# Kernel tuning notes

Measured on AMD Instinct MI355X. Metric: run time of the kernel, lower is better.

## Reference

```python
import jax, jax.numpy as jnp
import numpy as np

BATCH = 1024
LATENT = 16
IMG = 3 * 96 * 96  # 27648


def setup_inputs() -> dict:
    key = jax.random.key(0)
    ks = jax.random.split(key, 16)
    w = lambda k, shape, s=0.05: (jax.random.normal(k, shape, jnp.float32) * s)
    return {
        "x": jax.random.normal(ks[0], (BATCH, 96, 96, 3), jnp.float32),
        "eps_noise": jax.random.normal(ks[1], (BATCH, LATENT), jnp.float32),
        "enc_w1": w(ks[2], (IMG, 900)),
        "enc_b1": jnp.zeros((900,), jnp.float32),
        "enc_w2": w(ks[3], (900, 300)),
        "enc_b2": jnp.zeros((300,), jnp.float32),
        "logvar_w": w(ks[4], (300, LATENT)),
        "logvar_b": jnp.zeros((LATENT,), jnp.float32),
        "W": w(ks[5], (LATENT, LATENT), 0.1),  # nn.init.normal_(std=0.1)
        "dec_w1": w(ks[6], (LATENT, 300)),
        "dec_b1": jnp.zeros((300,), jnp.float32),
        "dec_w2": w(ks[7], (300, 300)),
        "dec_b2": jnp.zeros((300,), jnp.float32),
        "dec_w3": w(ks[8], (300, IMG)),
        "dec_b3": jnp.zeros((IMG,), jnp.float32),
    }


def reference(x, eps_noise, enc_w1, enc_b1, enc_w2, enc_b2, logvar_w, logvar_b,
              W, dec_w1, dec_b1, dec_w2, dec_b2, dec_w3, dec_b3):
    # encoder
    xf = x.reshape(x.shape[0], -1)                      # [B, 27648]
    h = jax.nn.elu(xf @ enc_w1 + enc_b1)
    h = jax.nn.elu(h @ enc_w2 + enc_b2)
    logvar = h @ logvar_w + logvar_b                    # [B, d]

    d = W.shape[0]
    idx = jnp.arange(d, dtype=W.dtype)
    relu_y = jnp.maximum(idx[None, :] - idx[:, None], 0.0)  # ReLU(j - i), strictly upper tri
    Bmat = W * relu_y                                    # strictly upper triangular

    # latent generating process: z_j = sum_{i<j} z_i B[i,j] + eps_j  <=>  z (I - B) = eps
    eps = jnp.exp(logvar / 2.0) * eps_noise             # [B, d]
    A = jnp.eye(d, dtype=W.dtype) - Bmat                # upper triangular
    # solve A^T z^T = eps^T (forward substitution), one fused triangular solve
    z = jax.scipy.linalg.solve_triangular(A, eps.T, trans=1, lower=False).T
    Bz = z @ Bmat                                       # equals per-column z[:, :j] @ B[:j, j]

    # decoder
    g = jax.nn.elu(z @ dec_w1 + dec_b1)
    g = jax.nn.elu(g @ dec_w2 + dec_b2)
    xhat = jnp.tanh(g @ dec_w3 + dec_b3).reshape(-1, 96, 96, 3)
    return z, logvar, Bz, Bmat, xhat
```

## Files before the change

### kernel.cpp

```cpp
#include <hip/hip_runtime.h>
#include <math.h>

#define ACT_NONE 0
#define ACT_ELU  1
#define ACT_TANH 2

typedef unsigned short u16;
typedef unsigned int   u32;
typedef __attribute__((ext_vector_type(8))) short short8;
typedef __attribute__((ext_vector_type(4))) float f32x4;

__device__ __forceinline__ float eluf(float v) { return v > 0.f ? v : __expf(v) - 1.f; }
__device__ __forceinline__ float tanh_fast(float v) {
    float t = __expf(2.f * v);
    return 1.f - 2.f / (t + 1.f);
}
__device__ __forceinline__ u16 bf16_rne(float x) {
    u32 u = __float_as_uint(x);
    u32 r = u + 0x7FFFu + ((u >> 16) & 1u);
    return (u16)(r >> 16);
}

__global__ __launch_bounds__(256) void convT(
    const float* __restrict__ in, int K, int N,
    u16* __restrict__ outHi, u16* __restrict__ outLo, int ldo)
{
    __shared__ float tile[32][33];
    const int t  = threadIdx.x;
    const int kt = blockIdx.x * 32;
    const int nt = blockIdx.y * 32;
    {
        int r = t >> 3, c = (t & 7) * 4;
        int gk = kt + r;
        float4 v = {0.f, 0.f, 0.f, 0.f};
        if (gk < K) {
            const float* p = in + (size_t)gk * N + nt + c;
            if (nt + c + 3 < N) {
                v = *reinterpret_cast<const float4*>(p);
            } else {
                if (nt + c + 0 < N) v.x = p[0];
                if (nt + c + 1 < N) v.y = p[1];
                if (nt + c + 2 < N) v.z = p[2];
                if (nt + c + 3 < N) v.w = p[3];
            }
        }
        tile[r][c] = v.x; tile[r][c + 1] = v.y; tile[r][c + 2] = v.z; tile[r][c + 3] = v.w;
    }
    __syncthreads();
    {
        int r = t >> 3, c = (t & 7) * 4;
        ushort4 h, l;
        float f[4];
#pragma unroll
        for (int e = 0; e < 4; ++e) f[e] = tile[c + e][r];
        u16 hh[4], ll[4];
#pragma unroll
        for (int e = 0; e < 4; ++e) {
            hh[e] = bf16_rne(f[e]);
            float hf = __uint_as_float((u32)hh[e] << 16);
            ll[e] = bf16_rne(f[e] - hf);
        }
        h.x = hh[0]; h.y = hh[1]; h.z = hh[2]; h.w = hh[3];
        l.x = ll[0]; l.y = ll[1]; l.z = ll[2]; l.w = ll[3];
        size_t o = (size_t)(nt + r) * ldo + kt + c;
        *reinterpret_cast<ushort4*>(outHi + o) = h;
        *reinterpret_cast<ushort4*>(outLo + o) = l;
    }
}

template <int ACT, bool ATOMIC>
__global__ __launch_bounds__(256) void mgemm(
    const float* __restrict__ A, int lda,
    const u16* __restrict__ Bhi, const u16* __restrict__ Blo, int ldb,
    const float* __restrict__ bias,
    float* __restrict__ C, int ldc,
    int Ncols, int kChunk, int Ktot)
{
    __shared__ u16 As[2][128][40];
    __shared__ u16 Bs[2][128][40];

    const int tid  = threadIdx.x;
    const int m0   = blockIdx.y * 128;
    const int n0   = blockIdx.x * 128;
    const int kbeg = blockIdx.z * kChunk;
    const int kend = min(Ktot, kbeg + kChunk);

    const int w  = tid >> 6;
    const int wm = (w >> 1) * 64;
    const int wn = (w & 1) * 64;
    const int ln = tid & 63;
    const int fr = ln & 15;
    const int kh = ln >> 4;

    const int srow = tid >> 1;
    const int skq  = (tid & 1) * 16;

    f32x4 acc[4][4];
#pragma unroll
    for (int i = 0; i < 4; ++i)
#pragma unroll
        for (int j = 0; j < 4; ++j) {
            f32x4 z = {0.f, 0.f, 0.f, 0.f};
            acc[i][j] = z;
        }

    for (int k0 = kbeg; k0 < kend; k0 += 32) {
        {
            const float* p = A + (size_t)(m0 + srow) * lda + k0 + skq;
            alignas(16) float vv[16];
            *reinterpret_cast<float4*>(&vv[0])  = reinterpret_cast<const float4*>(p)[0];
            *reinterpret_cast<float4*>(&vv[4])  = reinterpret_cast<const float4*>(p)[1];
            *reinterpret_cast<float4*>(&vv[8])  = reinterpret_cast<const float4*>(p)[2];
            *reinterpret_cast<float4*>(&vv[12]) = reinterpret_cast<const float4*>(p)[3];
            alignas(16) u16 h[16], l[16];
#pragma unroll
            for (int e = 0; e < 16; ++e) {
                u16 hh = bf16_rne(vv[e]);
                h[e] = hh;
                float hf = __uint_as_float((u32)hh << 16);
                l[e] = bf16_rne(vv[e] - hf);
            }
            *reinterpret_cast<uint4*>(&As[0][srow][skq])     = *reinterpret_cast<uint4*>(&h[0]);
            *reinterpret_cast<uint4*>(&As[0][srow][skq + 8]) = *reinterpret_cast<uint4*>(&h[8]);
            *reinterpret_cast<uint4*>(&As[1][srow][skq])     = *reinterpret_cast<uint4*>(&l[0]);
            *reinterpret_cast<uint4*>(&As[1][srow][skq + 8]) = *reinterpret_cast<uint4*>(&l[8]);
        }
        {
            const u16* p = Bhi + (size_t)(n0 + srow) * ldb + k0 + skq;
            uint4 u0 = reinterpret_cast<const uint4*>(p)[0];
            uint4 u1 = reinterpret_cast<const uint4*>(p)[1];
            *reinterpret_cast<uint4*>(&Bs[0][srow][skq])     = u0;
            *reinterpret_cast<uint4*>(&Bs[0][srow][skq + 8]) = u1;
            const u16* q = Blo + (size_t)(n0 + srow) * ldb + k0 + skq;
            uint4 v0 = reinterpret_cast<const uint4*>(q)[0];
            uint4 v1 = reinterpret_cast<const uint4*>(q)[1];
            *reinterpret_cast<uint4*>(&Bs[1][srow][skq])     = v0;
            *reinterpret_cast<uint4*>(&Bs[1][srow][skq + 8]) = v1;
        }
        __syncthreads();

        short8 ah[4], al[4], bh[4], bl[4];
#pragma unroll
        for (int i = 0; i < 4; ++i) {
            ah[i] = *reinterpret_cast<const short8*>(&As[0][wm + i * 16 + fr][kh * 8]);
            al[i] = *reinterpret_cast<const short8*>(&As[1][wm + i * 16 + fr][kh * 8]);
        }
#pragma unroll
        for (int j = 0; j < 4; ++j) {
            bh[j] = *reinterpret_cast<const short8*>(&Bs[0][wn + j * 16 + fr][kh * 8]);
            bl[j] = *reinterpret_cast<const short8*>(&Bs[1][wn + j * 16 + fr][kh * 8]);
        }
#pragma unroll
        for (int i = 0; i < 4; ++i)
#pragma unroll
            for (int j = 0; j < 4; ++j) {
                acc[i][j] = __builtin_amdgcn_mfma_f32_16x16x32_bf16(ah[i], bh[j], acc[i][j], 0, 0, 0);
                acc[i][j] = __builtin_amdgcn_mfma_f32_16x16x32_bf16(ah[i], bl[j], acc[i][j], 0, 0, 0);
                acc[i][j] = __builtin_amdgcn_mfma_f32_16x16x32_bf16(al[i], bh[j], acc[i][j], 0, 0, 0);
            }
        __syncthreads();
    }

#pragma unroll
    for (int j = 0; j < 4; ++j) {
        const int col = n0 + wn + j * 16 + fr;
        float bv = 0.f;
        if (!ATOMIC) bv = bias[col];
#pragma unroll
        for (int i = 0; i < 4; ++i) {
            const int rowb = m0 + wm + i * 16 + kh * 4;
#pragma unroll
            for (int p = 0; p < 4; ++p) {
                float v = acc[i][j][p];
                const int row = rowb + p;
                if (ATOMIC) {
                    if (col < Ncols) atomicAdd(&C[(size_t)row * ldc + col], v);
                } else {
                    v += bv;
                    if (ACT == ACT_TANH) v = tanh_fast(v);
                    else if (ACT == ACT_ELU) v = eluf(v);
                    C[(size_t)row * ldc + col] = v;
                }
            }
        }
    }
}

__global__ __launch_bounds__(256) void zero_f32(float* __restrict__ p, int n)
{
    int i = blockIdx.x * 256 + threadIdx.x;
    if (i < n) p[i] = 0.f;
}

__global__ __launch_bounds__(256) void bias_elu_inplace(
    float* __restrict__ p, const float* __restrict__ bias, int n, int N)
{
    int i = blockIdx.x * 256 + threadIdx.x;
    if (i < n) p[i] = eluf(p[i] + bias[i % N]);
}

template <int ACT>
__global__ __launch_bounds__(256) void rowgemm(
    const float* __restrict__ A, int strideA,
    const float* __restrict__ W, const float* __restrict__ bias,
    float* __restrict__ out, int strideOut, int padWidth,
    int N, int K)
{
    __shared__ float Arow[928];
    const int m = blockIdx.x;
    const int t = threadIdx.x;
    for (int k = t; k < K; k += 256) Arow[k] = A[(size_t)m * strideA + k];
    __syncthreads();
    for (int n = t; n < padWidth; n += 256) {
        float s = 0.f;
        if (n < N) {
            s = bias[n];
            for (int k = 0; k < K; ++k) s = fmaf(Arow[k], W[(size_t)k * N + n], s);
            if (ACT == ACT_ELU) s = eluf(s);
        }
        out[(size_t)m * strideOut + n] = s;
    }
}

__global__ __launch_bounds__(256) void latent_kernel(
    const float* __restrict__ logvar,
    const float* __restrict__ eps_noise,
    const float* __restrict__ Wlat,
    float* __restrict__ z_ws,
    float* __restrict__ out)
{
    __shared__ float Bm[256];
    const int t = threadIdx.x;
    {
        int i = t >> 4, j = t & 15;
        float v = (j > i) ? Wlat[t] * (float)(j - i) : 0.f;
        Bm[t] = v;
        if (blockIdx.x == 0) out[49152 + t] = v;
    }
    __syncthreads();

    const int b = blockIdx.x * 256 + t;
    float lv[16], z[16];
#pragma unroll
    for (int j = 0; j < 16; ++j) lv[j] = logvar[b * 16 + j];
#pragma unroll
    for (int j = 0; j < 16; ++j) {
        float s = __expf(0.5f * fminf(lv[j], 80.f)) * eps_noise[b * 16 + j];
        for (int i = 0; i < j; ++i) s = fmaf(z[i], Bm[i * 16 + j], s);
        z[j] = s;
    }
#pragma unroll
    for (int j = 0; j < 16; ++j) {
        float bz = 0.f;
#pragma unroll
        for (int i = 0; i < 16; ++i) bz = fmaf(z[i], Bm[i * 16 + j], bz);
        out[b * 16 + j]         = z[j];
        out[16384 + b * 16 + j] = lv[j];
        out[32768 + b * 16 + j] = bz;
        z_ws[b * 16 + j] = z[j];
    }
}

extern "C" void kernel_launch(void* const* d_in, const int* in_sizes, int n_in,
                              void* d_out, int out_size, void* d_ws, size_t ws_size,
                              hipStream_t stream)
{
    const float* x       = (const float*)d_in[0];
    const float* eps_n   = (const float*)d_in[1];
    const float* enc_w1  = (const float*)d_in[2];
    const float* enc_b1  = (const float*)d_in[3];
    const float* enc_w2  = (const float*)d_in[4];
    const float* enc_b2  = (const float*)d_in[5];
    const float* lv_w    = (const float*)d_in[6];
    const float* lv_b    = (const float*)d_in[7];
    const float* Wlat    = (const float*)d_in[8];
    const float* dec_w1  = (const float*)d_in[9];
    const float* dec_b1  = (const float*)d_in[10];
    const float* dec_w2  = (const float*)d_in[11];
    const float* dec_b2  = (const float*)d_in[12];
    const float* dec_w3  = (const float*)d_in[13];
    const float* dec_b3  = (const float*)d_in[14];

    char* ws = (char*)d_ws;
    float* h1     = (float*)(ws + 0);
    float* h2     = (float*)(ws + 3686400);
    float* lv     = (float*)(ws + 4915200);
    float* zf     = (float*)(ws + 4980736);
    float* g1     = (float*)(ws + 5046272);
    float* g2     = (float*)(ws + 6275072);
    u16*   w1t_hi = (u16*)(ws + 7585792);
    u16*   w1t_lo = (u16*)(ws + 64208896);
    u16*   w3t_hi = (u16*)(ws + 120832000);
    u16*   w3t_lo = (u16*)(ws + 138526720);

    float* out = (float*)d_out;

    convT<<<dim3(864, 32), 256, 0, stream>>>(enc_w1, 27648, 900, w1t_hi, w1t_lo, 27648);
    convT<<<dim3(10, 864), 256, 0, stream>>>(dec_w3, 300, 27648, w3t_hi, w3t_lo, 320);

    zero_f32<<<3600, 256, 0, stream>>>(h1, 921600);

    mgemm<ACT_NONE, true><<<dim3(8, 8, 8), 256, 0, stream>>>(
        x, 27648, w1t_hi, w1t_lo, 27648, nullptr,
        h1, 900, 900, 3456, 27648);

    bias_elu_inplace<<<3600, 256, 0, stream>>>(h1, enc_b1, 921600, 900);

    rowgemm<ACT_ELU><<<1024, 256, 0, stream>>>(
        h1, 900, enc_w2, enc_b2, h2, 300, 300, 300, 900);

    rowgemm<ACT_NONE><<<1024, 256, 0, stream>>>(
        h2, 300, lv_w, lv_b, lv, 16, 16, 16, 300);

    latent_kernel<<<4, 256, 0, stream>>>(lv, eps_n, Wlat, zf, out);

    rowgemm<ACT_ELU><<<1024, 256, 0, stream>>>(
        zf, 16, dec_w1, dec_b1, g1, 300, 300, 300, 16);

    rowgemm<ACT_ELU><<<1024, 256, 0, stream>>>(
        g1, 300, dec_w2, dec_b2, g2, 320, 320, 300, 300);

    mgemm<ACT_TANH, false><<<dim3(216, 8, 1), 256, 0, stream>>>(
        g2, 320, w3t_hi, w3t_lo, 320, dec_b3,
        out + 49408, 27648, 27648, 320, 320);
}
```

Baseline: 959.5 us.

## Pre-split activations to bf16 hi/lo and prefetch next K tile in registers

Input x and the decoder activation g2 are now split into bf16 hi/lo arrays ahead of time: a separate kernel does x, and the dec_w2 rowgemm does g2 in its epilogue. The GEMM therefore loads bf16 A directly instead of converting fp32 tiles inside the inner loop. The GEMM also register-prefetches the next K tile while computing on the current one, and the encoder GEMM uses twice as many K-split blocks. The trade-off is an extra full pass over x (read fp32, write two bf16 arrays), a larger workspace, and more atomic adds from the wider split-K.

```diff
diff --git a/kernel.cpp b/kernel.cpp
--- a/kernel.cpp
+++ b/kernel.cpp
@@ -19,6 +19,26 @@
     u32 u = __float_as_uint(x);
     u32 r = u + 0x7FFFu + ((u >> 16) & 1u);
     return (u16)(r >> 16);
+}
+
+__global__ __launch_bounds__(256) void splitX(
+    const float* __restrict__ in, u16* __restrict__ hi, u16* __restrict__ lo, int n)
+{
+    int i = (blockIdx.x * 256 + threadIdx.x) * 8;
+    if (i >= n) return;
+    float4 v0 = reinterpret_cast<const float4*>(in + i)[0];
+    float4 v1 = reinterpret_cast<const float4*>(in + i)[1];
+    float f[8] = {v0.x, v0.y, v0.z, v0.w, v1.x, v1.y, v1.z, v1.w};
+    alignas(16) u16 h[8], l[8];
+#pragma unroll
+    for (int e = 0; e < 8; ++e) {
+        u16 hh = bf16_rne(f[e]);
+        h[e] = hh;
+        float hf = __uint_as_float((u32)hh << 16);
+        l[e] = bf16_rne(f[e] - hf);
+    }
+    *reinterpret_cast<uint4*>(hi + i) = *reinterpret_cast<uint4*>(&h[0]);
+    *reinterpret_cast<uint4*>(lo + i) = *reinterpret_cast<uint4*>(&l[0]);
 }
 
 __global__ __launch_bounds__(256) void convT(
@@ -69,8 +89,8 @@
 }
 
 template <int ACT, bool ATOMIC>
-__global__ __launch_bounds__(256) void mgemm(
-    const float* __restrict__ A, int lda,
+__global__ __launch_bounds__(256) void mgemm2(
+    const u16* __restrict__ Ahi, const u16* __restrict__ Alo, int lda,
     const u16* __restrict__ Bhi, const u16* __restrict__ Blo, int ldb,
     const float* __restrict__ bias,
     float* __restrict__ C, int ldc,
@@ -95,6 +115,23 @@
     const int srow = tid >> 1;
     const int skq  = (tid & 1) * 16;
 
+    const u16* pAh = Ahi + (size_t)(m0 + srow) * lda + skq;
+    const u16* pAl = Alo + (size_t)(m0 + srow) * lda + skq;
+    const u16* pBh = Bhi + (size_t)(n0 + srow) * ldb + skq;
+    const u16* pBl = Blo + (size_t)(n0 + srow) * ldb + skq;
+
+    uint4 r0, r1, r2, r3, r4, r5, r6, r7;
+#define LOADK(kk) do {                                                   \
+        r0 = *reinterpret_cast<const uint4*>(pAh + (kk));                \
+        r1 = *reinterpret_cast<const uint4*>(pAh + (kk) + 8);            \
+        r2 = *reinterpret_cast<const uint4*>(pAl + (kk));                \
+        r3 = *reinterpret_cast<const uint4*>(pAl + (kk) + 8);            \
+        r4 = *reinterpret_cast<const uint4*>(pBh + (kk));                \
+        r5 = *reinterpret_cast<const uint4*>(pBh + (kk) + 8);            \
+        r6 = *reinterpret_cast<const uint4*>(pBl + (kk));                \
+        r7 = *reinterpret_cast<const uint4*>(pBl + (kk) + 8);            \
+    } while (0)
+
     f32x4 acc[4][4];
 #pragma unroll
     for (int i = 0; i < 4; ++i)
@@ -104,40 +141,19 @@
             acc[i][j] = z;
         }
 
+    LOADK(kbeg);
     for (int k0 = kbeg; k0 < kend; k0 += 32) {
-        {
-            const float* p = A + (size_t)(m0 + srow) * lda + k0 + skq;
-            alignas(16) float vv[16];
-            *reinterpret_cast<float4*>(&vv[0])  = reinterpret_cast<const float4*>(p)[0];
-            *reinterpret_cast<float4*>(&vv[4])  = reinterpret_cast<const float4*>(p)[1];
-            *reinterpret_cast<float4*>(&vv[8])  = reinterpret_cast<const float4*>(p)[2];
-            *reinterpret_cast<float4*>(&vv[12]) = reinterpret_cast<const float4*>(p)[3];
-            alignas(16) u16 h[16], l[16];
-#pragma unroll
-            for (int e = 0; e < 16; ++e) {
-                u16 hh = bf16_rne(vv[e]);
-                h[e] = hh;
-                float hf = __uint_as_float((u32)hh << 16);
-                l[e] = bf16_rne(vv[e] - hf);
-            }
-            *reinterpret_cast<uint4*>(&As[0][srow][skq])     = *reinterpret_cast<uint4*>(&h[0]);
-            *reinterpret_cast<uint4*>(&As[0][srow][skq + 8]) = *reinterpret_cast<uint4*>(&h[8]);
-            *reinterpret_cast<uint4*>(&As[1][srow][skq])     = *reinterpret_cast<uint4*>(&l[0]);
-            *reinterpret_cast<uint4*>(&As[1][srow][skq + 8]) = *reinterpret_cast<uint4*>(&l[8]);
-        }
-        {
-            const u16* p = Bhi + (size_t)(n0 + srow) * ldb + k0 + skq;
-            uint4 u0 = reinterpret_cast<const uint4*>(p)[0];
-            uint4 u1 = reinterpret_cast<const uint4*>(p)[1];
-            *reinterpret_cast<uint4*>(&Bs[0][srow][skq])     = u0;
-            *reinterpret_cast<uint4*>(&Bs[0][srow][skq + 8]) = u1;
-            const u16* q = Blo + (size_t)(n0 + srow) * ldb + k0 + skq;
-            uint4 v0 = reinterpret_cast<const uint4*>(q)[0];
-            uint4 v1 = reinterpret_cast<const uint4*>(q)[1];
-            *reinterpret_cast<uint4*>(&Bs[1][srow][skq])     = v0;
-            *reinterpret_cast<uint4*>(&Bs[1][srow][skq + 8]) = v1;
-        }
+        *reinterpret_cast<uint4*>(&As[0][srow][skq])     = r0;
+        *reinterpret_cast<uint4*>(&As[0][srow][skq + 8]) = r1;
+        *reinterpret_cast<uint4*>(&As[1][srow][skq])     = r2;
+        *reinterpret_cast<uint4*>(&As[1][srow][skq + 8]) = r3;
+        *reinterpret_cast<uint4*>(&Bs[0][srow][skq])     = r4;
+        *reinterpret_cast<uint4*>(&Bs[0][srow][skq + 8]) = r5;
+        *reinterpret_cast<uint4*>(&Bs[1][srow][skq])     = r6;
+        *reinterpret_cast<uint4*>(&Bs[1][srow][skq + 8]) = r7;
         __syncthreads();
+
+        if (k0 + 32 < kend) LOADK(k0 + 32);
 
         short8 ah[4], al[4], bh[4], bl[4];
 #pragma unroll
@@ -160,6 +176,7 @@
             }
         __syncthreads();
     }
+#undef LOADK
 
 #pragma unroll
     for (int j = 0; j < 4; ++j) {
@@ -219,6 +236,32 @@
             if (ACT == ACT_ELU) s = eluf(s);
         }
         out[(size_t)m * strideOut + n] = s;
+    }
+}
+
+__global__ __launch_bounds__(256) void rowgemm_split(
+    const float* __restrict__ A, int strideA,
+    const float* __restrict__ W, const float* __restrict__ bias,
+    u16* __restrict__ outHi, u16* __restrict__ outLo, int strideOut, int padWidth,
+    int N, int K)
+{
+    __shared__ float Arow[928];
+    const int m = blockIdx.x;
+    const int t = threadIdx.x;
+    for (int k = t; k < K; k += 256) Arow[k] = A[(size_t)m * strideA + k];
+    __syncthreads();
+    for (int n = t; n < padWidth; n += 256) {
+        u16 hh = 0, ll = 0;
+        if (n < N) {
+            float s = bias[n];
+            for (int k = 0; k < K; ++k) s = fmaf(Arow[k], W[(size_t)k * N + n], s);
+            s = eluf(s);
+            hh = bf16_rne(s);
+            float hf = __uint_as_float((u32)hh << 16);
+            ll = bf16_rne(s - hf);
+        }
+        outHi[(size_t)m * strideOut + n] = hh;
+        outLo[(size_t)m * strideOut + n] = ll;
     }
 }
 
@@ -287,22 +330,27 @@
     float* lv     = (float*)(ws + 4915200);
     float* zf     = (float*)(ws + 4980736);
     float* g1     = (float*)(ws + 5046272);
-    float* g2     = (float*)(ws + 6275072);
-    u16*   w1t_hi = (u16*)(ws + 7585792);
-    u16*   w1t_lo = (u16*)(ws + 64208896);
-    u16*   w3t_hi = (u16*)(ws + 120832000);
-    u16*   w3t_lo = (u16*)(ws + 138526720);
+    u16*   g2hi   = (u16*)(ws + 6275072);
+    u16*   g2lo   = (u16*)(ws + 6930432);
+    u16*   xhi    = (u16*)(ws + 7585792);
+    u16*   xlo    = (u16*)(ws + 64208896);
+    u16*   w1t_hi = (u16*)(ws + 120832000);
+    u16*   w1t_lo = (u16*)(ws + 177455104);
+    u16*   w3t_hi = (u16*)(ws + 234078208);
+    u16*   w3t_lo = (u16*)(ws + 251772928);
 
     float* out = (float*)d_out;
+
+    splitX<<<13824, 256, 0, stream>>>(x, xhi, xlo, 28311552);
 
     convT<<<dim3(864, 32), 256, 0, stream>>>(enc_w1, 27648, 900, w1t_hi, w1t_lo, 27648);
     convT<<<dim3(10, 864), 256, 0, stream>>>(dec_w3, 300, 27648, w3t_hi, w3t_lo, 320);
 
     zero_f32<<<3600, 256, 0, stream>>>(h1, 921600);
 
-    mgemm<ACT_NONE, true><<<dim3(8, 8, 8), 256, 0, stream>>>(
-        x, 27648, w1t_hi, w1t_lo, 27648, nullptr,
-        h1, 900, 900, 3456, 27648);
+    mgemm2<ACT_NONE, true><<<dim3(8, 8, 16), 256, 0, stream>>>(
+        xhi, xlo, 27648, w1t_hi, w1t_lo, 27648, nullptr,
+        h1, 900, 900, 1728, 27648);
 
     bias_elu_inplace<<<3600, 256, 0, stream>>>(h1, enc_b1, 921600, 900);
 
@@ -317,10 +365,10 @@
     rowgemm<ACT_ELU><<<1024, 256, 0, stream>>>(
         zf, 16, dec_w1, dec_b1, g1, 300, 300, 300, 16);
 
-    rowgemm<ACT_ELU><<<1024, 256, 0, stream>>>(
-        g1, 300, dec_w2, dec_b2, g2, 320, 320, 300, 300);
-
-    mgemm<ACT_TANH, false><<<dim3(216, 8, 1), 256, 0, stream>>>(
-        g2, 320, w3t_hi, w3t_lo, 320, dec_b3,
+    rowgemm_split<<<1024, 256, 0, stream>>>(
+        g1, 300, dec_w2, dec_b2, g2hi, g2lo, 320, 320, 300, 300);
+
+    mgemm2<ACT_TANH, false><<<dim3(216, 8, 1), 256, 0, stream>>>(
+        g2hi, g2lo, 320, w3t_hi, w3t_lo, 320, dec_b3,
         out + 49408, 27648, 27648, 320, 320);
 }
```

New measurement: 969.7 us. Within noise of the previous version (+1.1%).
